# Performance work log

Hardware: AMD Instinct MI355X
Metric: run time of the kernel (lower is better)

## Reference

```python
import jax, jax.numpy as jnp
import numpy as np

SCALE_MIN, SCALE_MAX = 0.01, 10.0
LN_EPS = 1e-5

B, KIN, H, C = 32, 6144, 512, 5


def _kaiming_uniform(k, shape):
    # torch kaiming_uniform_(a=sqrt(5)) on (out,in): bound = 1/sqrt(fan_in)
    bound = 1.0 / np.sqrt(shape[1])
    return jax.random.uniform(k, shape, minval=-bound, maxval=bound, dtype=jnp.float32)


def setup_inputs() -> dict:
    key = jax.random.key(0)
    ks = jax.random.split(key, 16)
    inp = {"x": jax.random.normal(ks[0], (B, KIN), dtype=jnp.float32)}
    dims = [(H, KIN), (H, H), (H, H)]
    for i, (o, n) in enumerate(dims):
        inp[f"w{i}"] = _kaiming_uniform(ks[1 + 3 * i], (o, n))
        inp[f"t{i}"] = jax.random.uniform(ks[2 + 3 * i], (o, n), minval=-1.0, maxval=1.0, dtype=jnp.float32)
        inp[f"s{i}"] = jax.random.uniform(ks[3 + 3 * i], (o, n), minval=-2.0, maxval=0.0, dtype=jnp.float32)
        inp[f"g{i}"] = jnp.ones((o,), jnp.float32)
        inp[f"b{i}"] = jnp.zeros((o,), jnp.float32)
    inp["cw"] = _kaiming_uniform(ks[10], (C, H))
    cbound = 1.0 / np.sqrt(H)
    inp["cb"] = jax.random.uniform(ks[11], (C,), minval=-cbound, maxval=cbound, dtype=jnp.float32)
    return inp


def _wavelet_linear(h, w, t, sr):
    # h: (B, in), params: (out, in)
    scale = SCALE_MIN + (SCALE_MAX - SCALE_MIN) * jax.nn.sigmoid(sr)
    s = (h[:, None, :] - t[None]) / (scale[None] + 1e-8)  # (B, out, in)
    psi = (1.0 - s * s) * jnp.exp(-0.5 * s * s)  # mexican hat
    return jnp.einsum('boi,oi->bo', psi, w)


def _layer_norm(h, g, b):
    m = jnp.mean(h, axis=-1, keepdims=True)
    v = jnp.mean(jnp.square(h - m), axis=-1, keepdims=True)
    return (h - m) * jax.lax.rsqrt(v + LN_EPS) * g + b


def reference(x, w0, t0, s0, g0, b0, w1, t1, s1, g1, b1, w2, t2, s2, g2, b2, cw, cb):
    h = x
    for (w, t, sr, g, b) in [(w0, t0, s0, g0, b0), (w1, t1, s1, g1, b1), (w2, t2, s2, g2, b2)]:
        h = _layer_norm(jax.nn.silu(_wavelet_linear(h, w, t, sr)), g, b)
    return h @ cw.T + cb
```

## Files before the change

### kernel.cpp

```cpp
#include <hip/hip_runtime.h>

#define LN_EPS 1e-5f
#define LOG2E 1.44269504f
#define NHALF_LOG2E (-0.72134752f)

#if __has_builtin(__builtin_amdgcn_exp2f)
#define EXP2F(x) __builtin_amdgcn_exp2f(x)
#else
#define EXP2F(x) __expf((x) * 0.69314718f)
#endif

typedef float v2f __attribute__((ext_vector_type(2)));

template<int KIN>
__global__ __launch_bounds__(256)
void transpose_x(const float* __restrict__ x, float* __restrict__ xT)
{
    int idx = blockIdx.x * 256 + threadIdx.x;
    int i = idx >> 5, b = idx & 31;
    xT[idx] = x[b * KIN + i];
}

template<int KIN, int S>
__global__ __launch_bounds__(128, 8)
void wav_layer(const float* __restrict__ xT, const float* __restrict__ w,
               const float* __restrict__ t, const float* __restrict__ s,
               float* __restrict__ part)
{
    constexpr int RANGE = KIN / S;
    constexpr int STEPS = RANGE / 4;
    constexpr int PREPS = RANGE / 64;
    __shared__ float2 prepA[2][RANGE];
    __shared__ float  prepW[2][RANGE];

    const int wave = threadIdx.x >> 6;
    const int lane = threadIdx.x & 63;
    const int o    = (blockIdx.x << 1) + wave;
    const int si   = blockIdx.y;
    const int ibase = si * RANGE;

    const float* __restrict__ wp = w + (size_t)o * KIN + ibase;
    const float* __restrict__ tp = t + (size_t)o * KIN + ibase;
    const float* __restrict__ sp = s + (size_t)o * KIN + ibase;

#pragma unroll
    for (int r = 0; r < PREPS; ++r) {
        int il = r * 64 + lane;
        float wv = wp[il], tv = tp[il], sv = sp[il];
        float sig = __builtin_amdgcn_rcpf(1.f + EXP2F(-sv * LOG2E));
        float inv = __builtin_amdgcn_rcpf(fmaf(9.99f, sig, 0.01000001f));
        prepA[wave][il] = make_float2(inv, -tv * inv);
        prepW[wave][il] = wv;
    }
    __syncthreads();

    const int p = lane & 15, g = lane >> 4;
    const v2f* __restrict__ xp = (const v2f*)xT + (size_t)(ibase + g) * 16 + p;

    v2f acc = {0.f, 0.f};
#pragma unroll 8
    for (int st = 0; st < STEPS; ++st) {
        float2 pr = prepA[wave][st * 4 + g];
        float  wj = prepW[wave][st * 4 + g];
        v2f xv = xp[(size_t)st * 64];
        v2f invv = {pr.x, pr.x};
        v2f ntiv = {pr.y, pr.y};
        v2f u  = __builtin_elementwise_fma(xv, invv, ntiv);
        v2f q  = u * u;
        v2f arg = q * (v2f){NHALF_LOG2E, NHALF_LOG2E};
        v2f ev = {EXP2F(arg.x), EXP2F(arg.y)};
        v2f wv2 = {wj, wj};
        v2f pw = __builtin_elementwise_fma(-wv2, q, wv2);
        acc = __builtin_elementwise_fma(pw, ev, acc);
    }

    float acc0 = acc.x, acc1 = acc.y;
    acc0 += __shfl_down(acc0, 32); acc0 += __shfl_down(acc0, 16);
    acc1 += __shfl_down(acc1, 32); acc1 += __shfl_down(acc1, 16);
    if (lane < 16) {
        float2* pp = (float2*)(part + (size_t)si * 16384 + o * 32) + p;
        *pp = make_float2(acc0, acc1);
    }
}

template<int S>
__global__ __launch_bounds__(512)
void silu_ln(const float* __restrict__ part, const float* __restrict__ g,
             const float* __restrict__ bias, float* __restrict__ hT)
{
    const int b = blockIdx.x, tid = threadIdx.x;
    float v = 0.f;
#pragma unroll
    for (int si = 0; si < S; ++si) v += part[(size_t)si * 16384 + tid * 32 + b];
    float a = v * __builtin_amdgcn_rcpf(1.f + EXP2F(-v * LOG2E));

    float s1 = a, s2 = a * a;
#pragma unroll
    for (int off = 32; off; off >>= 1) {
        s1 += __shfl_down(s1, off);
        s2 += __shfl_down(s2, off);
    }
    __shared__ float r1[8], r2[8];
    const int lane = tid & 63, wid = tid >> 6;
    if (lane == 0) { r1[wid] = s1; r2[wid] = s2; }
    __syncthreads();
    float t1 = 0.f, t2 = 0.f;
#pragma unroll
    for (int k = 0; k < 8; ++k) { t1 += r1[k]; t2 += r2[k]; }
    float m   = t1 * (1.f / 512.f);
    float var = t2 * (1.f / 512.f) - m * m;
    float r   = __builtin_amdgcn_rsqf(var + LN_EPS);
    hT[tid * 32 + b] = (a - m) * r * g[tid] + bias[tid];
}

template<int S>
__global__ __launch_bounds__(512)
void silu_ln_cls(const float* __restrict__ part, const float* __restrict__ g,
                 const float* __restrict__ bias, const float* __restrict__ cw,
                 const float* __restrict__ cb, float* __restrict__ out)
{
    const int b = blockIdx.x, tid = threadIdx.x;
    float v = 0.f;
#pragma unroll
    for (int si = 0; si < S; ++si) v += part[(size_t)si * 16384 + tid * 32 + b];
    float a = v * __builtin_amdgcn_rcpf(1.f + EXP2F(-v * LOG2E));

    float s1 = a, s2 = a * a;
#pragma unroll
    for (int off = 32; off; off >>= 1) {
        s1 += __shfl_down(s1, off);
        s2 += __shfl_down(s2, off);
    }
    __shared__ float r1[8], r2[8];
    const int lane = tid & 63, wid = tid >> 6;
    if (lane == 0) { r1[wid] = s1; r2[wid] = s2; }
    __syncthreads();
    float t1 = 0.f, t2 = 0.f;
#pragma unroll
    for (int k = 0; k < 8; ++k) { t1 += r1[k]; t2 += r2[k]; }
    float m   = t1 * (1.f / 512.f);
    float var = t2 * (1.f / 512.f) - m * m;
    float r   = __builtin_amdgcn_rsqf(var + LN_EPS);
    float hl  = (a - m) * r * g[tid] + bias[tid];

    __shared__ float cr[5][8];
#pragma unroll
    for (int c = 0; c < 5; ++c) {
        float pv = hl * cw[c * 512 + tid];
#pragma unroll
        for (int off = 32; off; off >>= 1) pv += __shfl_down(pv, off);
        if (lane == 0) cr[c][wid] = pv;
    }
    __syncthreads();
    if (tid < 5) {
        float sum = 0.f;
#pragma unroll
        for (int k = 0; k < 8; ++k) sum += cr[tid][k];
        out[b * 5 + tid] = sum + cb[tid];
    }
}

extern "C" void kernel_launch(void* const* d_in, const int* in_sizes, int n_in,
                              void* d_out, int out_size, void* d_ws, size_t ws_size,
                              hipStream_t stream)
{
    const float* x  = (const float*)d_in[0];
    const float* w0 = (const float*)d_in[1];
    const float* t0 = (const float*)d_in[2];
    const float* s0 = (const float*)d_in[3];
    const float* g0 = (const float*)d_in[4];
    const float* b0 = (const float*)d_in[5];
    const float* w1 = (const float*)d_in[6];
    const float* t1 = (const float*)d_in[7];
    const float* s1 = (const float*)d_in[8];
    const float* b1 = (const float*)d_in[10];
    const float* g1 = (const float*)d_in[9];
    const float* w2 = (const float*)d_in[11];
    const float* t2 = (const float*)d_in[12];
    const float* s2 = (const float*)d_in[13];
    const float* g2 = (const float*)d_in[14];
    const float* b2 = (const float*)d_in[15];
    const float* cw = (const float*)d_in[16];
    const float* cb = (const float*)d_in[17];
    float* out = (float*)d_out;

    float* xT   = (float*)d_ws;
    float* part = xT + 196608;
    float* hT   = part + 16 * 16384;

    transpose_x<6144><<<768, 256, 0, stream>>>(x, xT);
    wav_layer<6144, 16><<<dim3(256, 16), 128, 0, stream>>>(xT, w0, t0, s0, part);
    silu_ln<16><<<32, 512, 0, stream>>>(part, g0, b0, hT);
    wav_layer<512, 8><<<dim3(256, 8), 128, 0, stream>>>(hT, w1, t1, s1, part);
    silu_ln<8><<<32, 512, 0, stream>>>(part, g1, b1, hT);
    wav_layer<512, 8><<<dim3(256, 8), 128, 0, stream>>>(hT, w2, t2, s2, part);
    silu_ln_cls<8><<<32, 512, 0, stream>>>(part, g2, b2, cw, cb, out);
}
```

Baseline: 167.7 us.

## Process multiple outputs per wave reusing register-cached x across splits

```diff
diff --git a/kernel.cpp b/kernel.cpp
--- a/kernel.cpp
+++ b/kernel.cpp
@@ -21,65 +21,64 @@
     xT[idx] = x[b * KIN + i];
 }
 
-template<int KIN, int S>
-__global__ __launch_bounds__(128, 8)
+template<int KIN, int S, int NO>
+__global__ __launch_bounds__(128, 4)
 void wav_layer(const float* __restrict__ xT, const float* __restrict__ w,
                const float* __restrict__ t, const float* __restrict__ s,
                float* __restrict__ part)
 {
     constexpr int RANGE = KIN / S;
     constexpr int STEPS = RANGE / 4;
-    constexpr int PREPS = RANGE / 64;
-    __shared__ float2 prepA[2][RANGE];
-    __shared__ float  prepW[2][RANGE];
+    __shared__ float2 prepA[2][NO][RANGE];
+    __shared__ float  prepW[2][NO][RANGE];
 
-    const int wave = threadIdx.x >> 6;
-    const int lane = threadIdx.x & 63;
-    const int o    = (blockIdx.x << 1) + wave;
-    const int si   = blockIdx.y;
+    const int wave  = threadIdx.x >> 6;
+    const int lane  = threadIdx.x & 63;
+    const int obase = ((blockIdx.x << 1) + wave) * NO;
+    const int si    = blockIdx.y;
     const int ibase = si * RANGE;
 
-    const float* __restrict__ wp = w + (size_t)o * KIN + ibase;
-    const float* __restrict__ tp = t + (size_t)o * KIN + ibase;
-    const float* __restrict__ sp = s + (size_t)o * KIN + ibase;
-
 #pragma unroll
-    for (int r = 0; r < PREPS; ++r) {
-        int il = r * 64 + lane;
-        float wv = wp[il], tv = tp[il], sv = sp[il];
+    for (int e = lane; e < NO * RANGE; e += 64) {
+        int ol = e / RANGE, il = e - ol * RANGE;
+        size_t gi = (size_t)(obase + ol) * KIN + ibase + il;
+        float wv = w[gi], tv = t[gi], sv = s[gi];
         float sig = __builtin_amdgcn_rcpf(1.f + EXP2F(-sv * LOG2E));
         float inv = __builtin_amdgcn_rcpf(fmaf(9.99f, sig, 0.01000001f));
-        prepA[wave][il] = make_float2(inv, -tv * inv);
-        prepW[wave][il] = wv;
+        prepA[wave][ol][il] = make_float2(inv, -tv * inv);
+        prepW[wave][ol][il] = wv;
     }
     __syncthreads();
 
     const int p = lane & 15, g = lane >> 4;
     const v2f* __restrict__ xp = (const v2f*)xT + (size_t)(ibase + g) * 16 + p;
 
-    v2f acc = {0.f, 0.f};
-#pragma unroll 8
-    for (int st = 0; st < STEPS; ++st) {
-        float2 pr = prepA[wave][st * 4 + g];
-        float  wj = prepW[wave][st * 4 + g];
-        v2f xv = xp[(size_t)st * 64];
-        v2f invv = {pr.x, pr.x};
-        v2f ntiv = {pr.y, pr.y};
-        v2f u  = __builtin_elementwise_fma(xv, invv, ntiv);
-        v2f q  = u * u;
-        v2f arg = q * (v2f){NHALF_LOG2E, NHALF_LOG2E};
-        v2f ev = {EXP2F(arg.x), EXP2F(arg.y)};
-        v2f wv2 = {wj, wj};
-        v2f pw = __builtin_elementwise_fma(-wv2, q, wv2);
-        acc = __builtin_elementwise_fma(pw, ev, acc);
-    }
+    v2f xr[STEPS];
+#pragma unroll
+    for (int st = 0; st < STEPS; ++st) xr[st] = xp[(size_t)st * 64];
 
-    float acc0 = acc.x, acc1 = acc.y;
-    acc0 += __shfl_down(acc0, 32); acc0 += __shfl_down(acc0, 16);
-    acc1 += __shfl_down(acc1, 32); acc1 += __shfl_down(acc1, 16);
-    if (lane < 16) {
-        float2* pp = (float2*)(part + (size_t)si * 16384 + o * 32) + p;
-        *pp = make_float2(acc0, acc1);
+#pragma unroll
+    for (int ol = 0; ol < NO; ++ol) {
+        v2f acc = {0.f, 0.f};
+#pragma unroll
+        for (int st = 0; st < STEPS; ++st) {
+            float2 pr = prepA[wave][ol][st * 4 + g];
+            float  wj = prepW[wave][ol][st * 4 + g];
+            v2f u  = __builtin_elementwise_fma(xr[st], (v2f){pr.x, pr.x},
+                                               (v2f){pr.y, pr.y});
+            v2f q  = u * u;
+            v2f ev = {EXP2F(q.x * NHALF_LOG2E), EXP2F(q.y * NHALF_LOG2E)};
+            v2f pw = __builtin_elementwise_fma((v2f){-wj, -wj}, q,
+                                               (v2f){wj, wj});
+            acc = __builtin_elementwise_fma(pw, ev, acc);
+        }
+        float a0 = acc.x, a1 = acc.y;
+        a0 += __shfl_down(a0, 32); a0 += __shfl_down(a0, 16);
+        a1 += __shfl_down(a1, 32); a1 += __shfl_down(a1, 16);
+        if (lane < 16) {
+            float2* pp = (float2*)(part + (size_t)si * 16384 + (obase + ol) * 32) + p;
+            *pp = make_float2(a0, a1);
+        }
     }
 }
 
@@ -173,8 +172,8 @@
     const float* w1 = (const float*)d_in[6];
     const float* t1 = (const float*)d_in[7];
     const float* s1 = (const float*)d_in[8];
+    const float* g1 = (const float*)d_in[9];
     const float* b1 = (const float*)d_in[10];
-    const float* g1 = (const float*)d_in[9];
     const float* w2 = (const float*)d_in[11];
     const float* t2 = (const float*)d_in[12];
     const float* s2 = (const float*)d_in[13];
@@ -186,13 +185,13 @@
 
     float* xT   = (float*)d_ws;
     float* part = xT + 196608;
-    float* hT   = part + 16 * 16384;
+    float* hT   = part + 64 * 16384;
 
     transpose_x<6144><<<768, 256, 0, stream>>>(x, xT);
-    wav_layer<6144, 16><<<dim3(256, 16), 128, 0, stream>>>(xT, w0, t0, s0, part);
-    silu_ln<16><<<32, 512, 0, stream>>>(part, g0, b0, hT);
-    wav_layer<512, 8><<<dim3(256, 8), 128, 0, stream>>>(hT, w1, t1, s1, part);
-    silu_ln<8><<<32, 512, 0, stream>>>(part, g1, b1, hT);
-    wav_layer<512, 8><<<dim3(256, 8), 128, 0, stream>>>(hT, w2, t2, s2, part);
-    silu_ln_cls<8><<<32, 512, 0, stream>>>(part, g2, b2, cw, cb, out);
+    wav_layer<6144, 64, 8><<<dim3(32, 64), 128, 0, stream>>>(xT, w0, t0, s0, part);
+    silu_ln<64><<<32, 512, 0, stream>>>(part, g0, b0, hT);
+    wav_layer<512, 16, 4><<<dim3(64, 16), 128, 0, stream>>>(hT, w1, t1, s1, part);
+    silu_ln<16><<<32, 512, 0, stream>>>(part, g1, b1, hT);
+    wav_layer<512, 16, 4><<<dim3(64, 16), 128, 0, stream>>>(hT, w2, t2, s2, part);
+    silu_ln_cls<16><<<32, 512, 0, stream>>>(part, g2, b2, cw, cb, out);
 }
```

New measurement: 196.9 us. +17.4%, slower.
